# Kernel tuning notes

Measured on AMD Instinct MI355X. Metric: run time of the kernel, lower is better.

Reference implementation:

```python
import jax, jax.numpy as jnp
import numpy as np


def setup_inputs() -> dict:
    key = jax.random.key(0)
    inp = jax.random.normal(key, (8, 3, 224, 224), dtype=jnp.float32)
    return {"inp": inp, "tau_min": 1, "tau_max": 60, "ntau": 8,
            "num_angles": 12, "stride": 2}


def _logpolar_offsets(tau_min, tau_max, ntau, num_angles):
    # Matches the torch module: theta in [-pi, pi), tau logarithmically spaced,
    # coords stacked angle-major as (y, x) pairs (theta unsqueeze(1) outer).
    c = (tau_max / tau_min) ** (1.0 / (ntau - 1)) - 1.0
    theta = np.arange(num_angles, dtype=np.float64) * (2.0 * np.pi / num_angles) - np.pi
    tau = tau_min * (1.0 + c) ** np.arange(ntau, dtype=np.float64)
    x = tau[None, :] * np.cos(theta[:, None])   # (A, T)
    y = tau[None, :] * np.sin(theta[:, None])   # (A, T)
    return (jnp.asarray(y.ravel(), jnp.float32),
            jnp.asarray(x.ravel(), jnp.float32))  # each (A*T,)


def reference(inp, tau_min, tau_max, ntau, num_angles, stride):
    yoff, xoff = _logpolar_offsets(tau_min, tau_max, ntau, num_angles)
    B, F, H, W = inp.shape
    Hs = (H - 1) // stride + 1
    Ws = (W - 1) // stride + 1
    gy = jnp.arange(Hs, dtype=jnp.float32) * stride   # focus-point rows
    gx = jnp.arange(Ws, dtype=jnp.float32) * stride   # focus-point cols

    def sample(yo, xo):
        # Bilinear sample of inp at (i*stride + yo, j*stride + xo), zero outside.
        yq = gy + yo
        xq = gx + xo
        y0 = jnp.floor(yq)
        x0 = jnp.floor(xq)
        wy = (yq - y0)  # (Hs,)
        wx = (xq - x0)  # (Ws,)
        y0i = y0.astype(jnp.int32)
        x0i = x0.astype(jnp.int32)

        def gather(yi, xi):
            vy = ((yi >= 0) & (yi < H)).astype(inp.dtype)
            vx = ((xi >= 0) & (xi < W)).astype(inp.dtype)
            g = inp[:, :, jnp.clip(yi, 0, H - 1), :][:, :, :, jnp.clip(xi, 0, W - 1)]
            return g * (vy[:, None] * vx[None, :])  # (B,F,Hs,Ws)

        w00 = (1 - wy)[:, None] * (1 - wx)[None, :]
        w01 = (1 - wy)[:, None] * wx[None, :]
        w10 = wy[:, None] * (1 - wx)[None, :]
        w11 = wy[:, None] * wx[None, :]
        return (w00 * gather(y0i, x0i) + w01 * gather(y0i, x0i + 1)
                + w10 * gather(y0i + 1, x0i) + w11 * gather(y0i + 1, x0i + 1))

    out = jax.vmap(sample)(yoff, xoff)                    # (A*T, B, F, Hs, Ws)
    out = out.reshape(num_angles, ntau, B, F, Hs, Ws)
    out = jnp.transpose(out, (2, 3, 1, 0, 4, 5))          # (B, F, ntau, A, Hs, Ws)
    return out
```

## Files before the change

### kernel.cpp

```cpp
#include <hip/hip_runtime.h>
#include <cmath>
#include <algorithm>

#ifndef M_PI
#define M_PI 3.14159265358979323846
#endif

#define B_ 8
#define F_ 3
#define H_ 224
#define W_ 224
#define T_ 8
#define A_ 12
#define NK 96
#define STRIDE_ 2
#define HS_ 112
#define WS_ 112
#define PLANE_ (H_ * W_)
#define SLICE_ (HS_ * WS_)

#define RI 4
#define BANDMAX 70

struct LPArgs {
    int   cy[NK];  int cx[NK];
    float fy[NK];  float fx[NK];
    int   korig[NK];
    int   cymin[2]; int cymax[2];
};

static LPArgs make_args() {
    int cy[NK], cx[NK]; float fy[NK], fx[NK];
    double c = pow(60.0, 1.0 / 7.0) - 1.0;
    for (int t = 0; t < T_; ++t) {
        double tau = pow(1.0 + c, (double)t);
        for (int a = 0; a < A_; ++a) {
            double th = (double)a * (2.0 * M_PI / (double)A_) - M_PI;
            float yo = (float)(tau * sin(th)), xo = (float)(tau * cos(th));
            int k = t * A_ + a;
            float yf = floorf(yo), xf = floorf(xo);
            cy[k] = (int)yf; fy[k] = yo - yf;
            cx[k] = (int)xf; fx[k] = xo - xf;
        }
    }
    int idx[NK];
    for (int k = 0; k < NK; ++k) idx[k] = k;
    std::sort(idx, idx + NK, [&](int a, int b) { return cy[a] < cy[b]; });
    LPArgs r;
    r.cymin[0] = r.cymin[1] = 1000; r.cymax[0] = r.cymax[1] = -1000;
    for (int p = 0; p < NK; ++p) {
        int k = idx[p], g = p / 48;
        r.cy[p] = cy[k]; r.cx[p] = cx[k];
        r.fy[p] = fy[k]; r.fx[p] = fx[k];
        r.korig[p] = k;
        r.cymin[g] = std::min(r.cymin[g], cy[k]);
        r.cymax[g] = std::max(r.cymax[g], cy[k]);
    }
    return r;
}

__global__ __launch_bounds__(1024) void lp_sample_kernel(
    const float* __restrict__ inp, float* __restrict__ out, LPArgs args) {

    __shared__ float lds[BANDMAX * W_];

    const int bf = blockIdx.x;
    const int i0 = blockIdx.y * RI;
    const int g  = blockIdx.z;

    const int r0 = max(0, 2 * i0 + args.cymin[g]);
    const int r1 = min(H_ - 1, 2 * i0 + 2 * (RI - 1) + args.cymax[g] + 1);

    const float* plane = inp + (size_t)bf * PLANE_;
    {
        const float4* s4 = (const float4*)(plane + r0 * W_);
        float4*       d4 = (float4*)lds;
        const int n4 = (r1 - r0 + 1) * (W_ / 4);
        for (int v = threadIdx.x; v < n4; v += 1024) d4[v] = s4[v];
    }
    __syncthreads();

    const int lane = threadIdx.x & 63;
    const int wave = __builtin_amdgcn_readfirstlane(threadIdx.x >> 6);

    float* outp = out + (size_t)bf * (NK * SLICE_) + (size_t)i0 * WS_;

#pragma unroll 1
    for (int tt = 0; tt < 6; ++tt) {
        const int task = wave + (tt << 4);
        const int kl   = task >> 1;
        const int h    = task & 1;
        const int kk   = g * 48 + kl;

        const int   cy = args.cy[kk]; const float fy = args.fy[kk];
        const int   cx = args.cx[kk]; const float fx = args.fx[kk];
        const int   ko = args.korig[kk];

        const int j   = h * 64 + lane;
        const int ix0 = 2 * j + cx;
        float wA, wB;
        if (ix0 >= 0 && ix0 <= W_ - 2)  { wA = 1.0f - fx; wB = fx; }
        else if (ix0 == -1)             { wA = fx;        wB = 0.0f; }
        else if (ix0 == W_ - 1)         { wA = 0.0f;      wB = 1.0f - fx; }
        else                            { wA = 0.0f;      wB = 0.0f; }
        const int bx = min(max(ix0, 0), W_ - 2);
        const float* lcol = lds + bx;

        float* orow = outp + (size_t)ko * SLICE_ + j;
        const bool act = (j < WS_);

#pragma unroll
        for (int di = 0; di < RI; ++di) {
            const int iy0 = 2 * (i0 + di) + cy;
            float mA, mB;
            if (iy0 >= 0 && iy0 <= H_ - 2)  { mA = 1.0f - fy; mB = fy; }
            else if (iy0 == -1)             { mA = fy;        mB = 0.0f; }
            else if (iy0 == H_ - 1)         { mA = 0.0f;      mB = 1.0f - fy; }
            else                            { mA = 0.0f;      mB = 0.0f; }
            const int by = min(max(iy0, 0), H_ - 2);

            const float* p = lcol + (by - r0) * W_;
            float g00 = p[0],   g01 = p[1];
            float g10 = p[W_],  g11 = p[W_ + 1];

            float r = mA * (wA * g00 + wB * g01)
                    + mB * (wA * g10 + wB * g11);

            if (act) orow[(size_t)di * WS_] = r;
        }
    }
}

extern "C" void kernel_launch(void* const* d_in, const int* in_sizes, int n_in,
                              void* d_out, int out_size, void* d_ws, size_t ws_size,
                              hipStream_t stream) {
    const float* inp = (const float*)d_in[0];
    float*       out = (float*)d_out;

    static const LPArgs args = make_args();

    dim3 grid(B_ * F_, HS_ / RI, 2);
    lp_sample_kernel<<<grid, 1024, 0, stream>>>(inp, out, args);
}
```

Baseline: 133.3 us.

## Deinterleave LDS rows by column parity and double rows per block

Stores each staged input row in LDS split into even and odd columns with a padded pitch, so stride-2 lanes read consecutive addresses instead of conflicting banks. Doubles the output rows per block, which halves the grid and amortizes the band load over more rows. It also adds an occupancy hint to the launch bounds and reworks the horizontal edge weights for the split layout. The cost is more scalar stores during staging and a larger LDS footprint per block.

```diff
diff --git a/kernel.cpp b/kernel.cpp
--- a/kernel.cpp
+++ b/kernel.cpp
@@ -19,8 +19,10 @@
 #define PLANE_ (H_ * W_)
 #define SLICE_ (HS_ * WS_)
 
-#define RI 4
-#define BANDMAX 70
+#define RI 8
+#define BANDROWS 78
+#define PITCH 225
+#define HALF 112
 
 struct LPArgs {
     int   cy[NK];  int cx[NK];
@@ -59,10 +61,10 @@
     return r;
 }
 
-__global__ __launch_bounds__(1024) void lp_sample_kernel(
+__global__ __launch_bounds__(1024, 8) void lp_sample_kernel(
     const float* __restrict__ inp, float* __restrict__ out, LPArgs args) {
 
-    __shared__ float lds[BANDMAX * W_];
+    __shared__ float lds[BANDROWS * PITCH];
 
     const int bf = blockIdx.x;
     const int i0 = blockIdx.y * RI;
@@ -70,13 +72,23 @@
 
     const int r0 = max(0, 2 * i0 + args.cymin[g]);
     const int r1 = min(H_ - 1, 2 * i0 + 2 * (RI - 1) + args.cymax[g] + 1);
+    const int nrows = min(r1 - r0 + 1, BANDROWS);
 
     const float* plane = inp + (size_t)bf * PLANE_;
+
     {
-        const float4* s4 = (const float4*)(plane + r0 * W_);
-        float4*       d4 = (float4*)lds;
-        const int n4 = (r1 - r0 + 1) * (W_ / 4);
-        for (int v = threadIdx.x; v < n4; v += 1024) d4[v] = s4[v];
+        const int n = nrows * (W_ / 4);
+        for (int v = threadIdx.x; v < n; v += 1024) {
+            const unsigned r = (unsigned)v / 56u;
+            const int u = v - (int)r * 56;
+            const float4 val = *(const float4*)(plane + (size_t)(r0 + (int)r) * W_ + 4 * u);
+            float* rowp = lds + r * PITCH;
+            const int e = 2 * u;
+            rowp[e]            = val.x;
+            rowp[e + 1]        = val.z;
+            rowp[HALF + e]     = val.y;
+            rowp[HALF + e + 1] = val.w;
+        }
     }
     __syncthreads();
 
@@ -95,38 +107,44 @@
         const int   cy = args.cy[kk]; const float fy = args.fy[kk];
         const int   cx = args.cx[kk]; const float fx = args.fx[kk];
         const int   ko = args.korig[kk];
+        const int   P  = cx & 1;
 
         const int j   = h * 64 + lane;
         const int ix0 = 2 * j + cx;
-        float wA, wB;
-        if (ix0 >= 0 && ix0 <= W_ - 2)  { wA = 1.0f - fx; wB = fx; }
-        else if (ix0 == -1)             { wA = fx;        wB = 0.0f; }
-        else if (ix0 == W_ - 1)         { wA = 0.0f;      wB = 1.0f - fx; }
-        else                            { wA = 0.0f;      wB = 0.0f; }
-        const int bx = min(max(ix0, 0), W_ - 2);
-        const float* lcol = lds + bx;
+        const float wLv = (ix0 >= 0  && ix0 <= W_ - 1) ? (1.0f - fx) : 0.0f;
+        const float wRv = (ix0 >= -1 && ix0 <= W_ - 2) ? fx          : 0.0f;
+        int eidx = (ix0 + P) >> 1;
+        int oidx = (ix0 + 1 - P) >> 1;
+        eidx = min(max(eidx, 0), HALF - 1);
+        oidx = min(max(oidx, 0), HALF - 1);
+        const float wE = P ? wRv : wLv;
+        const float wO = P ? wLv : wRv;
+
+        const float* eptr = lds + eidx;
+        const float* optr = lds + HALF + oidx;
 
         float* orow = outp + (size_t)ko * SLICE_ + j;
-        const bool act = (j < WS_);
 
-#pragma unroll
-        for (int di = 0; di < RI; ++di) {
-            const int iy0 = 2 * (i0 + di) + cy;
-            float mA, mB;
-            if (iy0 >= 0 && iy0 <= H_ - 2)  { mA = 1.0f - fy; mB = fy; }
-            else if (iy0 == -1)             { mA = fy;        mB = 0.0f; }
-            else if (iy0 == H_ - 1)         { mA = 0.0f;      mB = 1.0f - fy; }
-            else                            { mA = 0.0f;      mB = 0.0f; }
-            const int by = min(max(iy0, 0), H_ - 2);
+        if (j < WS_) {
+#pragma unroll 2
+            for (int di = 0; di < RI; ++di) {
+                const int iy0 = 2 * (i0 + di) + cy;
+                float mA, mB;
+                if (iy0 >= 0 && iy0 <= H_ - 2)  { mA = 1.0f - fy; mB = fy; }
+                else if (iy0 == -1)             { mA = fy;        mB = 0.0f; }
+                else if (iy0 == H_ - 1)         { mA = 0.0f;      mB = 1.0f - fy; }
+                else                            { mA = 0.0f;      mB = 0.0f; }
+                const int by = min(max(iy0, 0), H_ - 2);
+                const int rb = (by - r0) * PITCH;
 
-            const float* p = lcol + (by - r0) * W_;
-            float g00 = p[0],   g01 = p[1];
-            float g10 = p[W_],  g11 = p[W_ + 1];
+                const float e0 = eptr[rb], e1 = eptr[rb + PITCH];
+                const float o0 = optr[rb], o1 = optr[rb + PITCH];
 
-            float r = mA * (wA * g00 + wB * g01)
-                    + mB * (wA * g10 + wB * g11);
+                const float rr = wE * (mA * e0 + mB * e1)
+                               + wO * (mA * o0 + mB * o1);
 
-            if (act) orow[(size_t)di * WS_] = r;
+                orow[(size_t)di * WS_] = rr;
+            }
         }
     }
 }
```

Result: no change. 133.3 us (-0.0%).

## Replace LDS band staging with per-offset direct global gather kernel

Applied to the files above, without the earlier changes.

The LDS-staged kernel, which loaded a row band per block and looped over sorted offsets, is replaced by one block per (plane, offset) pair. Each block streams the whole 112x112 output slice contiguously and reads the input directly from global memory, relying on L2/L1 cache. A block-index swizzle groups blocks that share an input plane so they run together. This removes the LDS fill and barrier and makes the output writes fully contiguous, but each sample now makes four uncoalesced-ish global reads instead of reading from LDS.

```diff
diff --git a/kernel.cpp b/kernel.cpp
--- a/kernel.cpp
+++ b/kernel.cpp
@@ -1,6 +1,5 @@
 #include <hip/hip_runtime.h>
 #include <cmath>
-#include <algorithm>
 
 #ifndef M_PI
 #define M_PI 3.14159265358979323846
@@ -19,18 +18,14 @@
 #define PLANE_ (H_ * W_)
 #define SLICE_ (HS_ * WS_)
 
-#define RI 4
-#define BANDMAX 70
 
 struct LPArgs {
     int   cy[NK];  int cx[NK];
     float fy[NK];  float fx[NK];
-    int   korig[NK];
-    int   cymin[2]; int cymax[2];
 };
 
 static LPArgs make_args() {
-    int cy[NK], cx[NK]; float fy[NK], fx[NK];
+    LPArgs r;
     double c = pow(60.0, 1.0 / 7.0) - 1.0;
     for (int t = 0; t < T_; ++t) {
         double tau = pow(1.0 + c, (double)t);
@@ -39,95 +34,59 @@
             float yo = (float)(tau * sin(th)), xo = (float)(tau * cos(th));
             int k = t * A_ + a;
             float yf = floorf(yo), xf = floorf(xo);
-            cy[k] = (int)yf; fy[k] = yo - yf;
-            cx[k] = (int)xf; fx[k] = xo - xf;
+            r.cy[k] = (int)yf; r.fy[k] = yo - yf;
+            r.cx[k] = (int)xf; r.fx[k] = xo - xf;
         }
-    }
-    int idx[NK];
-    for (int k = 0; k < NK; ++k) idx[k] = k;
-    std::sort(idx, idx + NK, [&](int a, int b) { return cy[a] < cy[b]; });
-    LPArgs r;
-    r.cymin[0] = r.cymin[1] = 1000; r.cymax[0] = r.cymax[1] = -1000;
-    for (int p = 0; p < NK; ++p) {
-        int k = idx[p], g = p / 48;
-        r.cy[p] = cy[k]; r.cx[p] = cx[k];
-        r.fy[p] = fy[k]; r.fx[p] = fx[k];
-        r.korig[p] = k;
-        r.cymin[g] = std::min(r.cymin[g], cy[k]);
-        r.cymax[g] = std::max(r.cymax[g], cy[k]);
     }
     return r;
 }
 
-__global__ __launch_bounds__(1024) void lp_sample_kernel(
+__global__ __launch_bounds__(256) void lp_gather_kernel(
     const float* __restrict__ inp, float* __restrict__ out, LPArgs args) {
 
-    __shared__ float lds[BANDMAX * W_];
+    const int blk = (int)blockIdx.x;
+    const int swz = (blk & 7) * 288 + (blk >> 3);
+    const int bf  = swz / 96;
+    const int k   = swz - bf * 96;
 
-    const int bf = blockIdx.x;
-    const int i0 = blockIdx.y * RI;
-    const int g  = blockIdx.z;
+    const int   cy = args.cy[k];  const int   cx = args.cx[k];
+    const float fy = args.fy[k];  const float fx = args.fx[k];
+    const float omfy = 1.0f - fy, omfx = 1.0f - fx;
 
-    const int r0 = max(0, 2 * i0 + args.cymin[g]);
-    const int r1 = min(H_ - 1, 2 * i0 + 2 * (RI - 1) + args.cymax[g] + 1);
+    const float* plane  = inp + (size_t)bf * PLANE_;
+    float*       op     = out + ((size_t)bf * NK + k) * SLICE_ + threadIdx.x;
 
-    const float* plane = inp + (size_t)bf * PLANE_;
-    {
-        const float4* s4 = (const float4*)(plane + r0 * W_);
-        float4*       d4 = (float4*)lds;
-        const int n4 = (r1 - r0 + 1) * (W_ / 4);
-        for (int v = threadIdx.x; v < n4; v += 1024) d4[v] = s4[v];
-    }
-    __syncthreads();
-
-    const int lane = threadIdx.x & 63;
-    const int wave = __builtin_amdgcn_readfirstlane(threadIdx.x >> 6);
-
-    float* outp = out + (size_t)bf * (NK * SLICE_) + (size_t)i0 * WS_;
+    int i = (int)threadIdx.x / 112;
+    int j = (int)threadIdx.x - i * 112;
 
 #pragma unroll 1
-    for (int tt = 0; tt < 6; ++tt) {
-        const int task = wave + (tt << 4);
-        const int kl   = task >> 1;
-        const int h    = task & 1;
-        const int kk   = g * 48 + kl;
+    for (int it = 0; it < 49; ++it) {
+        const int y0 = 2 * i + cy;
+        const int x0 = 2 * j + cx;
 
-        const int   cy = args.cy[kk]; const float fy = args.fy[kk];
-        const int   cx = args.cx[kk]; const float fx = args.fx[kk];
-        const int   ko = args.korig[kk];
+        const float mA = (y0 >= 0  && y0 <  H_    ) ? omfy : 0.0f;
+        const float mB = (y0 >= -1 && y0 <  H_ - 1) ? fy   : 0.0f;
+        const float wA = (x0 >= 0  && x0 <  W_    ) ? omfx : 0.0f;
+        const float wB = (x0 >= -1 && x0 <  W_ - 1) ? fx   : 0.0f;
 
-        const int j   = h * 64 + lane;
-        const int ix0 = 2 * j + cx;
-        float wA, wB;
-        if (ix0 >= 0 && ix0 <= W_ - 2)  { wA = 1.0f - fx; wB = fx; }
-        else if (ix0 == -1)             { wA = fx;        wB = 0.0f; }
-        else if (ix0 == W_ - 1)         { wA = 0.0f;      wB = 1.0f - fx; }
-        else                            { wA = 0.0f;      wB = 0.0f; }
-        const int bx = min(max(ix0, 0), W_ - 2);
-        const float* lcol = lds + bx;
+        const int ya = min(max(y0,     0), H_ - 1);
+        const int yb = min(max(y0 + 1, 0), H_ - 1);
+        const int xa = min(max(x0,     0), W_ - 1);
+        const int xb = min(max(x0 + 1, 0), W_ - 1);
 
-        float* orow = outp + (size_t)ko * SLICE_ + j;
-        const bool act = (j < WS_);
+        const float* rA = plane + ya * W_;
+        const float* rB = plane + yb * W_;
+        const float g00 = rA[xa], g01 = rA[xb];
+        const float g10 = rB[xa], g11 = rB[xb];
 
-#pragma unroll
-        for (int di = 0; di < RI; ++di) {
-            const int iy0 = 2 * (i0 + di) + cy;
-            float mA, mB;
-            if (iy0 >= 0 && iy0 <= H_ - 2)  { mA = 1.0f - fy; mB = fy; }
-            else if (iy0 == -1)             { mA = fy;        mB = 0.0f; }
-            else if (iy0 == H_ - 1)         { mA = 0.0f;      mB = 1.0f - fy; }
-            else                            { mA = 0.0f;      mB = 0.0f; }
-            const int by = min(max(iy0, 0), H_ - 2);
+        const float rr = mA * (wA * g00 + wB * g01)
+                       + mB * (wA * g10 + wB * g11);
 
-            const float* p = lcol + (by - r0) * W_;
-            float g00 = p[0],   g01 = p[1];
-            float g10 = p[W_],  g11 = p[W_ + 1];
+        *op = rr;
+        op += 256;
 
-            float r = mA * (wA * g00 + wB * g01)
-                    + mB * (wA * g10 + wB * g11);
-
-            if (act) orow[(size_t)di * WS_] = r;
-        }
+        j += 32; i += 2;
+        if (j >= 112) { j -= 112; ++i; }
     }
 }
 
@@ -139,6 +98,5 @@
 
     static const LPArgs args = make_args();
 
-    dim3 grid(B_ * F_, HS_ / RI, 2);
-    lp_sample_kernel<<<grid, 1024, 0, stream>>>(inp, out, args);
+    lp_gather_kernel<<<dim3(B_ * F_ * NK), 256, 0, stream>>>(inp, out, args);
 }
```

New measurement: 176.7 us. +32.5%, slower.
